# Kernel optimization log

Hardware: AMD Instinct MI355X
Metric: run time of the kernel (lower is better)

## Reference

```python
import jax, jax.numpy as jnp
import numpy as np

N_NODES = 100000
HIDDEN = 128
N_EDGES = 1600000


def setup_inputs() -> dict:
    key = jax.random.key(0)
    k_z, k_e, k_w1, k_b1, k_w2, k_b2 = jax.random.split(key, 6)
    z = jax.random.normal(k_z, (N_NODES, HIDDEN), dtype=jnp.float32)
    edge_index = jax.random.randint(k_e, (2, N_EDGES), 0, N_NODES, dtype=jnp.int64)
    # torch.nn.Linear default init: U(-1/sqrt(fan_in), 1/sqrt(fan_in))
    lim1 = 1.0 / np.sqrt(2 * HIDDEN)
    W1 = jax.random.uniform(k_w1, (2 * HIDDEN, HIDDEN), minval=-lim1, maxval=lim1, dtype=jnp.float32)
    b1 = jax.random.uniform(k_b1, (HIDDEN,), minval=-lim1, maxval=lim1, dtype=jnp.float32)
    lim2 = 1.0 / np.sqrt(HIDDEN)
    W2 = jax.random.uniform(k_w2, (HIDDEN, 1), minval=-lim2, maxval=lim2, dtype=jnp.float32)
    b2 = jax.random.uniform(k_b2, (1,), minval=-lim2, maxval=lim2, dtype=jnp.float32)
    return {"z": z, "edge_index": edge_index, "W1": W1, "b1": b1, "W2": W2, "b2": b2}


def reference(z, edge_index, W1, b1, W2, b2):
    src = edge_index[0]
    dst = edge_index[1]
    # gather node pairs -> concat: [E, 2H]
    edge_feat = jnp.concatenate([z[src], z[dst]], axis=1)
    h = jax.nn.relu(edge_feat @ W1 + b1)  # [E, H]
    score = h @ W2 + b2                   # [E, 1]
    return score
```

## Files before the change

kernel.cpp:

```cpp
#include <hip/hip_runtime.h>
#include <hip/hip_bf16.h>
#include <stdint.h>

#define HIDDEN 128

typedef __attribute__((ext_vector_type(8))) short bf16x8;
typedef __attribute__((ext_vector_type(16))) float f32x16;

static __device__ __forceinline__ uint32_t cvt2(float a, float b) {
    union { __hip_bfloat162 h2; uint32_t u; } c;
    c.h2 = __float22bfloat162_rn(make_float2(a, b));
    return c.u;
}
static __device__ __forceinline__ float bf_lo(uint32_t p) {
    union { uint32_t u; float f; } v; v.u = p << 16; return v.f;
}
static __device__ __forceinline__ float bf_hi(uint32_t p) {
    union { uint32_t u; float f; } v; v.u = p & 0xffff0000u; return v.f;
}
static __device__ __forceinline__ bf16x8 pack8(float4 a, float4 b) {
    union { uint32_t u[4]; bf16x8 v; } r;
    r.u[0] = cvt2(a.x, a.y); r.u[1] = cvt2(a.z, a.w);
    r.u[2] = cvt2(b.x, b.y); r.u[3] = cvt2(b.z, b.w);
    return r.v;
}

__global__ __launch_bounds__(256) void transpose_w1(
    const float* __restrict__ W1, unsigned short* __restrict__ Wt)
{
    const int t = blockIdx.x * 256 + threadIdx.x;
    if (t >= 4096) return;
    const int cc = t >> 4;
    const int kg = t & 15;
    const int ccol = cc & 127;
    const int kofs = (cc >= 128) ? 128 : 0;
    uint32_t u[4];
    #pragma unroll
    for (int p = 0; p < 4; ++p) {
        const float a = W1[(size_t)(kofs + kg * 8 + 2 * p) * 128 + ccol];
        const float b = W1[(size_t)(kofs + kg * 8 + 2 * p + 1) * 128 + ccol];
        u[p] = cvt2(a, b);
    }
    uint4 o = { u[0], u[1], u[2], u[3] };
    *reinterpret_cast<uint4*>(Wt + (size_t)cc * 128 + kg * 8) = o;
}


struct ZBuf { float4 a[8], b[8]; };

static __device__ __forceinline__ void load_z(ZBuf& zb, const float* __restrict__ z,
                                              int ng, int nl, int hi, int n_nodes) {
    int node = ng * 32 + nl;
    node = (node < n_nodes) ? node : (n_nodes - 1);
    const float* zrow = z + (size_t)node * HIDDEN;
    #pragma unroll
    for (int ks = 0; ks < 8; ++ks) {
        zb.a[ks] = *reinterpret_cast<const float4*>(zrow + ks * 16 + hi * 8);
        zb.b[ks] = *reinterpret_cast<const float4*>(zrow + ks * 16 + hi * 8 + 4);
    }
}

static __device__ __forceinline__ void compute_to_lds(
    const ZBuf& zb, const bf16x8 (&wf)[2][8], const f32x16 (&binit)[2],
    char* Sm, int nl, int hi, int w)
{
    bf16x8 zf[8];
    #pragma unroll
    for (int ks = 0; ks < 8; ++ks) zf[ks] = pack8(zb.a[ks], zb.b[ks]);

    f32x16 acc0 = binit[0];
    f32x16 acc1 = binit[1];
    #pragma unroll
    for (int ks = 0; ks < 8; ++ks) {
        acc0 = __builtin_amdgcn_mfma_f32_32x32x16_bf16(wf[0][ks], zf[ks], acc0, 0, 0, 0);
        acc1 = __builtin_amdgcn_mfma_f32_32x32x16_bf16(wf[1][ks], zf[ks], acc1, 0, 0, 0);
    }

    const int swz = (nl & 15) << 3;
    #pragma unroll
    for (int g = 0; g < 4; ++g) {
        uint2 s0, s1;
        s0.x = cvt2(acc0[4 * g + 0], acc0[4 * g + 1]);
        s0.y = cvt2(acc0[4 * g + 2], acc0[4 * g + 3]);
        s1.x = cvt2(acc1[4 * g + 0], acc1[4 * g + 1]);
        s1.y = cvt2(acc1[4 * g + 2], acc1[4 * g + 3]);
        const int colb0 = w * 128 + g * 16 + hi * 8;
        const int colb1 = w * 128 + 64 + g * 16 + hi * 8;
        *reinterpret_cast<uint2*>(Sm + nl * 512 + (colb0 ^ swz)) = s0;
        *reinterpret_cast<uint2*>(Sm + nl * 512 + (colb1 ^ swz)) = s1;
    }
}

static __device__ __forceinline__ void copy_out(
    unsigned short* __restrict__ UV, const char* Sm, int ng, int tid, int n_nodes)
{
    const int colb0 = (tid & 31) * 16;
    #pragma unroll
    for (int rep = 0; rep < 4; ++rep) {
        const int node_local = rep * 8 + (tid >> 5);
        const int swz = (node_local & 15) << 3;
        const uint2 g0 = *reinterpret_cast<const uint2*>(Sm + node_local * 512 + ((colb0) ^ swz));
        const uint2 g1 = *reinterpret_cast<const uint2*>(Sm + node_local * 512 + ((colb0 + 8) ^ swz));
        const int node = ng * 32 + node_local;
        if (node < n_nodes) {
            uint4 o = { g0.x, g0.y, g1.x, g1.y };
            *reinterpret_cast<uint4*>(UV + (size_t)node * 256 + (tid & 31) * 8) = o;
        }
    }
}

__global__ __launch_bounds__(256) void precompute_mfma32(
    const float* __restrict__ z, const float* __restrict__ W1,
    const unsigned short* __restrict__ Wt,
    const float* __restrict__ b1,
    unsigned short* __restrict__ UV, int n_nodes, int n_groups)
{
    __shared__ char Sm[32 * 512];

    const int tid = threadIdx.x;
    const int lane = tid & 63;
    const int w = tid >> 6;
    const int nl = lane & 31;
    const int hi = lane >> 5;

    bf16x8 wf[2][8];
    if (Wt) {
        #pragma unroll
        for (int cg = 0; cg < 2; ++cg) {
            const int cc = w * 64 + cg * 32 + nl;
            #pragma unroll
            for (int ks = 0; ks < 8; ++ks) {
                const int k0 = ks * 16 + hi * 8;
                wf[cg][ks] = *reinterpret_cast<const bf16x8*>(Wt + (size_t)cc * 128 + k0);
            }
        }
    } else {
        #pragma unroll
        for (int cg = 0; cg < 2; ++cg) {
            const int cc = w * 64 + cg * 32 + nl;
            const int ccol = cc & 127;
            const int kofs = (cc >= 128) ? 128 : 0;
            #pragma unroll
            for (int ks = 0; ks < 8; ++ks) {
                const int k0 = ks * 16 + hi * 8 + kofs;
                float t[8];
                #pragma unroll
                for (int j = 0; j < 8; ++j)
                    t[j] = W1[(size_t)(k0 + j) * 128 + ccol];
                union { uint32_t u[4]; bf16x8 v; } fu;
                fu.u[0] = cvt2(t[0], t[1]); fu.u[1] = cvt2(t[2], t[3]);
                fu.u[2] = cvt2(t[4], t[5]); fu.u[3] = cvt2(t[6], t[7]);
                wf[cg][ks] = fu.v;
            }
        }
    }

    f32x16 binit[2];
    #pragma unroll
    for (int cg = 0; cg < 2; ++cg) {
        const int cc0 = w * 64 + cg * 32;
        #pragma unroll
        for (int r = 0; r < 16; ++r) {
            const int crow = (r & 3) + 8 * (r >> 2) + 4 * hi;
            const int cc = cc0 + crow;
            binit[cg][r] = (cc < 128) ? b1[cc] : 0.f;
        }
    }

    const int stride = gridDim.x;
    int ng = blockIdx.x;
    if (ng >= n_groups) return;

    ZBuf bufA, bufB;
    load_z(bufA, z, ng, nl, hi, n_nodes);

    while (ng < n_groups) {
        const int n1 = ng + stride;
        if (n1 < n_groups) load_z(bufB, z, n1, nl, hi, n_nodes);
        compute_to_lds(bufA, wf, binit, Sm, nl, hi, w);
        __syncthreads();
        copy_out(UV, Sm, ng, tid, n_nodes);
        __syncthreads();
        if (n1 >= n_groups) break;

        const int n2 = n1 + stride;
        if (n2 < n_groups) load_z(bufA, z, n2, nl, hi, n_nodes);
        compute_to_lds(bufB, wf, binit, Sm, nl, hi, w);
        __syncthreads();
        copy_out(UV, Sm, n1, tid, n_nodes);
        __syncthreads();
        ng = n2;
    }
}

static __device__ __forceinline__ float dot8(uint4 u, uint4 v, const float* w) {
    const uint32_t up[4] = { u.x, u.y, u.z, u.w };
    const uint32_t vp[4] = { v.x, v.y, v.z, v.w };
    float s = 0.f;
    #pragma unroll
    for (int p = 0; p < 4; ++p) {
        const float h0 = bf_lo(up[p]) + bf_lo(vp[p]);
        const float h1 = bf_hi(up[p]) + bf_hi(vp[p]);
        s = fmaf(fmaxf(h0, 0.f), w[2 * p], s);
        s = fmaf(fmaxf(h1, 0.f), w[2 * p + 1], s);
    }
    return s;
}
static __device__ __forceinline__ float red16(float s) {
    s += __shfl_xor(s, 1, 64); s += __shfl_xor(s, 2, 64);
    s += __shfl_xor(s, 4, 64); s += __shfl_xor(s, 8, 64);
    return s;
}

#define EPG 8

__global__ __launch_bounds__(256, 4) void edge_score(
    const int* __restrict__ ei, const unsigned short* __restrict__ UV,
    const float* __restrict__ W2, const float* __restrict__ b2,
    float* __restrict__ out, int n_edges)
{
    const int g = (blockIdx.x * 256 + threadIdx.x) >> 4;
    const int q = threadIdx.x & 15;
    const int e0 = g * EPG;
    if (e0 >= n_edges) return;

    const float4 w2a = *reinterpret_cast<const float4*>(W2 + q * 8);
    const float4 w2b = *reinterpret_cast<const float4*>(W2 + q * 8 + 4);
    const float wloc[8] = { w2a.x, w2a.y, w2a.z, w2a.w, w2b.x, w2b.y, w2b.z, w2b.w };
    const float bias = b2[0];

    const char* UVb = (const char*)UV;
    const uint32_t qo = (uint32_t)q * 16u;

    if (e0 + EPG - 1 < n_edges) {
        const int4 sA = *reinterpret_cast<const int4*>(ei + e0);
        const int4 sB = *reinterpret_cast<const int4*>(ei + e0 + 4);
        const int4 dA = *reinterpret_cast<const int4*>(ei + n_edges + e0);
        const int4 dB = *reinterpret_cast<const int4*>(ei + n_edges + e0 + 4);
        const int sidx[EPG] = { sA.x, sA.y, sA.z, sA.w, sB.x, sB.y, sB.z, sB.w };
        const int didx[EPG] = { dA.x, dA.y, dA.z, dA.w, dB.x, dB.y, dB.z, dB.w };

        uint4 u[EPG], v[EPG];
        #pragma unroll
        for (int i = 0; i < EPG; ++i) {
            u[i] = *reinterpret_cast<const uint4*>(UVb + ((uint32_t)sidx[i] * 512u + qo));
            v[i] = *reinterpret_cast<const uint4*>(UVb + ((uint32_t)didx[i] * 512u + 256u + qo));
        }
        __builtin_amdgcn_sched_barrier(0);

        float s[EPG];
        #pragma unroll
        for (int i = 0; i < EPG; ++i) s[i] = dot8(u[i], v[i], wloc);
        #pragma unroll
        for (int i = 0; i < EPG; ++i) s[i] = red16(s[i]) + bias;

        if (q == 0) {
            float4 oA = { s[0], s[1], s[2], s[3] };
            float4 oB = { s[4], s[5], s[6], s[7] };
            *reinterpret_cast<float4*>(out + e0) = oA;
            *reinterpret_cast<float4*>(out + e0 + 4) = oB;
        }
    } else {
        for (int i = 0; i < EPG; ++i) {
            const int e = e0 + i;
            if (e >= n_edges) break;
            const int si = ei[e];
            const int di = ei[n_edges + e];
            const uint4 uu = *reinterpret_cast<const uint4*>(UVb + ((uint32_t)si * 512u + qo));
            const uint4 vv = *reinterpret_cast<const uint4*>(UVb + ((uint32_t)di * 512u + 256u + qo));
            float s = red16(dot8(uu, vv, wloc));
            if (q == 0) out[e] = s + bias;
        }
    }
}

extern "C" void kernel_launch(void* const* d_in, const int* in_sizes, int n_in,
                              void* d_out, int out_size, void* d_ws, size_t ws_size,
                              hipStream_t stream) {
    const float* z  = (const float*)d_in[0];
    const int*   ei = (const int*)d_in[1];
    const float* W1 = (const float*)d_in[2];
    const float* b1 = (const float*)d_in[3];
    const float* W2 = (const float*)d_in[4];
    const float* b2 = (const float*)d_in[5];
    float* out = (float*)d_out;

    const int n_nodes = in_sizes[0] / HIDDEN;
    const int n_edges = in_sizes[1] / 2;

    unsigned short* UV = (unsigned short*)d_ws;
    const size_t uv_bytes = (size_t)n_nodes * 256 * sizeof(unsigned short);

    unsigned short* Wt = nullptr;
    if (ws_size >= uv_bytes + 256 * 128 * sizeof(unsigned short))
        Wt = UV + (size_t)n_nodes * 256;

    if (Wt) transpose_w1<<<16, 256, 0, stream>>>(W1, Wt);

    {
        const int n_groups = (n_nodes + 31) / 32;
        const int g1 = n_groups < 512 ? n_groups : 512;
        precompute_mfma32<<<g1, 256, 0, stream>>>(z, W1, Wt, b1, UV, n_nodes, n_groups);
    }
    {
        const int groups = (n_edges + EPG - 1) / EPG;
        const int blocks = (groups * 16 + 255) / 256;
        edge_score<<<blocks, 256, 0, stream>>>(ei, UV, W2, b2, out, n_edges);
    }
}
```

Before: 152.9 us.

## Stage z through LDS with coalesced loads and move b1 add to edge kernel

The node precompute kernel now loads z rows cooperatively with coalesced 64-byte-per-thread reads, converts them to bf16, and stages them in a swizzled LDS tile that the MFMA fragments read from. This replaces per-lane strided register double-buffering and cuts the prefetch register footprint. The b1 bias is no longer folded into the MFMA accumulators but added per edge in the scoring kernel, and the precompute grid grows from 512 to 768 blocks. In exchange there is an extra LDS round trip and barrier per group, and some extra per-edge adds. Adding b1 after U and V are rounded to bf16 also shifts rounding slightly.

```diff
diff --git a/kernel.cpp b/kernel.cpp
--- a/kernel.cpp
+++ b/kernel.cpp
@@ -17,12 +17,6 @@
 }
 static __device__ __forceinline__ float bf_hi(uint32_t p) {
     union { uint32_t u; float f; } v; v.u = p & 0xffff0000u; return v.f;
-}
-static __device__ __forceinline__ bf16x8 pack8(float4 a, float4 b) {
-    union { uint32_t u[4]; bf16x8 v; } r;
-    r.u[0] = cvt2(a.x, a.y); r.u[1] = cvt2(a.z, a.w);
-    r.u[2] = cvt2(b.x, b.y); r.u[3] = cvt2(b.z, b.w);
-    return r.v;
 }
 
 __global__ __launch_bounds__(256) void transpose_w1(
@@ -46,75 +40,13 @@
 }
 
 
-struct ZBuf { float4 a[8], b[8]; };
-
-static __device__ __forceinline__ void load_z(ZBuf& zb, const float* __restrict__ z,
-                                              int ng, int nl, int hi, int n_nodes) {
-    int node = ng * 32 + nl;
-    node = (node < n_nodes) ? node : (n_nodes - 1);
-    const float* zrow = z + (size_t)node * HIDDEN;
-    #pragma unroll
-    for (int ks = 0; ks < 8; ++ks) {
-        zb.a[ks] = *reinterpret_cast<const float4*>(zrow + ks * 16 + hi * 8);
-        zb.b[ks] = *reinterpret_cast<const float4*>(zrow + ks * 16 + hi * 8 + 4);
-    }
-}
-
-static __device__ __forceinline__ void compute_to_lds(
-    const ZBuf& zb, const bf16x8 (&wf)[2][8], const f32x16 (&binit)[2],
-    char* Sm, int nl, int hi, int w)
-{
-    bf16x8 zf[8];
-    #pragma unroll
-    for (int ks = 0; ks < 8; ++ks) zf[ks] = pack8(zb.a[ks], zb.b[ks]);
-
-    f32x16 acc0 = binit[0];
-    f32x16 acc1 = binit[1];
-    #pragma unroll
-    for (int ks = 0; ks < 8; ++ks) {
-        acc0 = __builtin_amdgcn_mfma_f32_32x32x16_bf16(wf[0][ks], zf[ks], acc0, 0, 0, 0);
-        acc1 = __builtin_amdgcn_mfma_f32_32x32x16_bf16(wf[1][ks], zf[ks], acc1, 0, 0, 0);
-    }
-
-    const int swz = (nl & 15) << 3;
-    #pragma unroll
-    for (int g = 0; g < 4; ++g) {
-        uint2 s0, s1;
-        s0.x = cvt2(acc0[4 * g + 0], acc0[4 * g + 1]);
-        s0.y = cvt2(acc0[4 * g + 2], acc0[4 * g + 3]);
-        s1.x = cvt2(acc1[4 * g + 0], acc1[4 * g + 1]);
-        s1.y = cvt2(acc1[4 * g + 2], acc1[4 * g + 3]);
-        const int colb0 = w * 128 + g * 16 + hi * 8;
-        const int colb1 = w * 128 + 64 + g * 16 + hi * 8;
-        *reinterpret_cast<uint2*>(Sm + nl * 512 + (colb0 ^ swz)) = s0;
-        *reinterpret_cast<uint2*>(Sm + nl * 512 + (colb1 ^ swz)) = s1;
-    }
-}
-
-static __device__ __forceinline__ void copy_out(
-    unsigned short* __restrict__ UV, const char* Sm, int ng, int tid, int n_nodes)
-{
-    const int colb0 = (tid & 31) * 16;
-    #pragma unroll
-    for (int rep = 0; rep < 4; ++rep) {
-        const int node_local = rep * 8 + (tid >> 5);
-        const int swz = (node_local & 15) << 3;
-        const uint2 g0 = *reinterpret_cast<const uint2*>(Sm + node_local * 512 + ((colb0) ^ swz));
-        const uint2 g1 = *reinterpret_cast<const uint2*>(Sm + node_local * 512 + ((colb0 + 8) ^ swz));
-        const int node = ng * 32 + node_local;
-        if (node < n_nodes) {
-            uint4 o = { g0.x, g0.y, g1.x, g1.y };
-            *reinterpret_cast<uint4*>(UV + (size_t)node * 256 + (tid & 31) * 8) = o;
-        }
-    }
-}
 
 __global__ __launch_bounds__(256) void precompute_mfma32(
     const float* __restrict__ z, const float* __restrict__ W1,
     const unsigned short* __restrict__ Wt,
-    const float* __restrict__ b1,
     unsigned short* __restrict__ UV, int n_nodes, int n_groups)
 {
+    __shared__ char Zt[32 * 256];
     __shared__ char Sm[32 * 512];
 
     const int tid = threadIdx.x;
@@ -123,16 +55,21 @@
     const int nl = lane & 31;
     const int hi = lane >> 5;
 
+    const int st_node = tid >> 3;
+    const int st_j2 = tid & 7;
+    const int st_swz = (st_node & 7) << 4;
+    const int st_addrA = st_node * 256 + ((st_j2 * 32) ^ st_swz);
+    const int st_addrB = st_node * 256 + ((st_j2 * 32 + 16) ^ st_swz);
+
     bf16x8 wf[2][8];
     if (Wt) {
         #pragma unroll
         for (int cg = 0; cg < 2; ++cg) {
             const int cc = w * 64 + cg * 32 + nl;
             #pragma unroll
-            for (int ks = 0; ks < 8; ++ks) {
-                const int k0 = ks * 16 + hi * 8;
-                wf[cg][ks] = *reinterpret_cast<const bf16x8*>(Wt + (size_t)cc * 128 + k0);
-            }
+            for (int ks = 0; ks < 8; ++ks)
+                wf[cg][ks] = *reinterpret_cast<const bf16x8*>(
+                    Wt + (size_t)cc * 128 + ks * 16 + hi * 8);
         }
     } else {
         #pragma unroll
@@ -155,52 +92,109 @@
         }
     }
 
-    f32x16 binit[2];
-    #pragma unroll
-    for (int cg = 0; cg < 2; ++cg) {
-        const int cc0 = w * 64 + cg * 32;
-        #pragma unroll
-        for (int r = 0; r < 16; ++r) {
-            const int crow = (r & 3) + 8 * (r >> 2) + 4 * hi;
-            const int cc = cc0 + crow;
-            binit[cg][r] = (cc < 128) ? b1[cc] : 0.f;
-        }
-    }
-
     const int stride = gridDim.x;
     int ng = blockIdx.x;
     if (ng >= n_groups) return;
 
-    ZBuf bufA, bufB;
-    load_z(bufA, z, ng, nl, hi, n_nodes);
+    float4 nz0, nz1, nz2, nz3;
+    {
+        int node = ng * 32 + st_node;
+        node = (node < n_nodes) ? node : (n_nodes - 1);
+        const float* zp = z + (size_t)node * HIDDEN + st_j2 * 16;
+        nz0 = *reinterpret_cast<const float4*>(zp);
+        nz1 = *reinterpret_cast<const float4*>(zp + 4);
+        nz2 = *reinterpret_cast<const float4*>(zp + 8);
+        nz3 = *reinterpret_cast<const float4*>(zp + 12);
+    }
 
     while (ng < n_groups) {
-        const int n1 = ng + stride;
-        if (n1 < n_groups) load_z(bufB, z, n1, nl, hi, n_nodes);
-        compute_to_lds(bufA, wf, binit, Sm, nl, hi, w);
+        {
+            uint4 A, B;
+            A.x = cvt2(nz0.x, nz0.y); A.y = cvt2(nz0.z, nz0.w);
+            A.z = cvt2(nz1.x, nz1.y); A.w = cvt2(nz1.z, nz1.w);
+            B.x = cvt2(nz2.x, nz2.y); B.y = cvt2(nz2.z, nz2.w);
+            B.z = cvt2(nz3.x, nz3.y); B.w = cvt2(nz3.z, nz3.w);
+            *reinterpret_cast<uint4*>(Zt + st_addrA) = A;
+            *reinterpret_cast<uint4*>(Zt + st_addrB) = B;
+        }
+
+        const int ngn = ng + stride;
+        if (ngn < n_groups) {
+            int node = ngn * 32 + st_node;
+            node = (node < n_nodes) ? node : (n_nodes - 1);
+            const float* zp = z + (size_t)node * HIDDEN + st_j2 * 16;
+            nz0 = *reinterpret_cast<const float4*>(zp);
+            nz1 = *reinterpret_cast<const float4*>(zp + 4);
+            nz2 = *reinterpret_cast<const float4*>(zp + 8);
+            nz3 = *reinterpret_cast<const float4*>(zp + 12);
+        }
+
         __syncthreads();
-        copy_out(UV, Sm, ng, tid, n_nodes);
+
+        {
+            const int rd_swz = (nl & 7) << 4;
+            bf16x8 zf[8];
+            #pragma unroll
+            for (int ks = 0; ks < 8; ++ks) {
+                const int off = ks * 32 + hi * 16;
+                zf[ks] = *reinterpret_cast<const bf16x8*>(
+                    Zt + nl * 256 + (off ^ rd_swz));
+            }
+
+            f32x16 acc0 = {};
+            f32x16 acc1 = {};
+            #pragma unroll
+            for (int ks = 0; ks < 8; ++ks) {
+                acc0 = __builtin_amdgcn_mfma_f32_32x32x16_bf16(wf[0][ks], zf[ks], acc0, 0, 0, 0);
+                acc1 = __builtin_amdgcn_mfma_f32_32x32x16_bf16(wf[1][ks], zf[ks], acc1, 0, 0, 0);
+            }
+
+            const int swz = (nl & 15) << 3;
+            #pragma unroll
+            for (int g = 0; g < 4; ++g) {
+                uint2 s0, s1;
+                s0.x = cvt2(acc0[4 * g + 0], acc0[4 * g + 1]);
+                s0.y = cvt2(acc0[4 * g + 2], acc0[4 * g + 3]);
+                s1.x = cvt2(acc1[4 * g + 0], acc1[4 * g + 1]);
+                s1.y = cvt2(acc1[4 * g + 2], acc1[4 * g + 3]);
+                const int colb0 = w * 128 + g * 16 + hi * 8;
+                const int colb1 = w * 128 + 64 + g * 16 + hi * 8;
+                *reinterpret_cast<uint2*>(Sm + nl * 512 + (colb0 ^ swz)) = s0;
+                *reinterpret_cast<uint2*>(Sm + nl * 512 + (colb1 ^ swz)) = s1;
+            }
+        }
+
         __syncthreads();
-        if (n1 >= n_groups) break;
-
-        const int n2 = n1 + stride;
-        if (n2 < n_groups) load_z(bufA, z, n2, nl, hi, n_nodes);
-        compute_to_lds(bufB, wf, binit, Sm, nl, hi, w);
-        __syncthreads();
-        copy_out(UV, Sm, n1, tid, n_nodes);
-        __syncthreads();
-        ng = n2;
-    }
-}
-
-static __device__ __forceinline__ float dot8(uint4 u, uint4 v, const float* w) {
+
+        {
+            const int colb0 = (tid & 31) * 16;
+            #pragma unroll
+            for (int rep = 0; rep < 4; ++rep) {
+                const int node_local = rep * 8 + (tid >> 5);
+                const int swz = (node_local & 15) << 3;
+                const uint2 g0 = *reinterpret_cast<const uint2*>(Sm + node_local * 512 + ((colb0) ^ swz));
+                const uint2 g1 = *reinterpret_cast<const uint2*>(Sm + node_local * 512 + ((colb0 + 8) ^ swz));
+                const int node = ng * 32 + node_local;
+                if (node < n_nodes) {
+                    uint4 o = { g0.x, g0.y, g1.x, g1.y };
+                    *reinterpret_cast<uint4*>(UV + (size_t)node * 256 + (tid & 31) * 8) = o;
+                }
+            }
+        }
+
+        ng = ngn;
+    }
+}
+
+static __device__ __forceinline__ float dot8(uint4 u, uint4 v,
+                                             const float* w, const float* bb) {
     const uint32_t up[4] = { u.x, u.y, u.z, u.w };
     const uint32_t vp[4] = { v.x, v.y, v.z, v.w };
     float s = 0.f;
     #pragma unroll
     for (int p = 0; p < 4; ++p) {
-        const float h0 = bf_lo(up[p]) + bf_lo(vp[p]);
-        const float h1 = bf_hi(up[p]) + bf_hi(vp[p]);
+        const float h0 = bf_lo(up[p]) + bf_lo(vp[p]) + bb[2 * p];
+        const float h1 = bf_hi(up[p]) + bf_hi(vp[p]) + bb[2 * p + 1];
         s = fmaf(fmaxf(h0, 0.f), w[2 * p], s);
         s = fmaf(fmaxf(h1, 0.f), w[2 * p + 1], s);
     }
@@ -216,8 +210,8 @@
 
 __global__ __launch_bounds__(256, 4) void edge_score(
     const int* __restrict__ ei, const unsigned short* __restrict__ UV,
-    const float* __restrict__ W2, const float* __restrict__ b2,
-    float* __restrict__ out, int n_edges)
+    const float* __restrict__ b1, const float* __restrict__ W2,
+    const float* __restrict__ b2, float* __restrict__ out, int n_edges)
 {
     const int g = (blockIdx.x * 256 + threadIdx.x) >> 4;
     const int q = threadIdx.x & 15;
@@ -227,6 +221,9 @@
     const float4 w2a = *reinterpret_cast<const float4*>(W2 + q * 8);
     const float4 w2b = *reinterpret_cast<const float4*>(W2 + q * 8 + 4);
     const float wloc[8] = { w2a.x, w2a.y, w2a.z, w2a.w, w2b.x, w2b.y, w2b.z, w2b.w };
+    const float4 b1a = *reinterpret_cast<const float4*>(b1 + q * 8);
+    const float4 b1b = *reinterpret_cast<const float4*>(b1 + q * 8 + 4);
+    const float bb[8] = { b1a.x, b1a.y, b1a.z, b1a.w, b1b.x, b1b.y, b1b.z, b1b.w };
     const float bias = b2[0];
 
     const char* UVb = (const char*)UV;
@@ -250,7 +247,7 @@
 
         float s[EPG];
         #pragma unroll
-        for (int i = 0; i < EPG; ++i) s[i] = dot8(u[i], v[i], wloc);
+        for (int i = 0; i < EPG; ++i) s[i] = dot8(u[i], v[i], wloc, bb);
         #pragma unroll
         for (int i = 0; i < EPG; ++i) s[i] = red16(s[i]) + bias;
 
@@ -268,7 +265,7 @@
             const int di = ei[n_edges + e];
             const uint4 uu = *reinterpret_cast<const uint4*>(UVb + ((uint32_t)si * 512u + qo));
             const uint4 vv = *reinterpret_cast<const uint4*>(UVb + ((uint32_t)di * 512u + 256u + qo));
-            float s = red16(dot8(uu, vv, wloc));
+            float s = red16(dot8(uu, vv, wloc, bb));
             if (q == 0) out[e] = s + bias;
         }
     }
@@ -299,12 +296,12 @@
 
     {
         const int n_groups = (n_nodes + 31) / 32;
-        const int g1 = n_groups < 512 ? n_groups : 512;
-        precompute_mfma32<<<g1, 256, 0, stream>>>(z, W1, Wt, b1, UV, n_nodes, n_groups);
+        const int g1 = n_groups < 768 ? n_groups : 768;
+        precompute_mfma32<<<g1, 256, 0, stream>>>(z, W1, Wt, UV, n_nodes, n_groups);
     }
     {
         const int groups = (n_edges + EPG - 1) / EPG;
         const int blocks = (groups * 16 + 255) / 256;
-        edge_score<<<blocks, 256, 0, stream>>>(ei, UV, W2, b2, out, n_edges);
-    }
-}
+        edge_score<<<blocks, 256, 0, stream>>>(ei, UV, b1, W2, b2, out, n_edges);
+    }
+}
```

After: 133.8 us. -12.5%, faster.
